# Performance work log

Measured on AMD Instinct MI355X. Metric: run time of the kernel, lower is better.

Reference implementation:

```python
import jax, jax.numpy as jnp
import numpy as np

EPS_PROJ = 4e-3   # geoopt float32 ball projection eps
ATANH_EPS = 1e-7

def artanh(x):
    return jnp.arctanh(jnp.clip(x, -1.0 + ATANH_EPS, 1.0 - ATANH_EPS))

def project(x):
    norm = jnp.linalg.norm(x, axis=-1, keepdims=True)
    maxnorm = 1.0 - EPS_PROJ
    return jnp.where(norm > maxnorm, x * (maxnorm / jnp.maximum(norm, 1e-15)), x)

def expmap0(u):
    un = jnp.linalg.norm(u, axis=-1, keepdims=True)
    return jnp.tanh(un) * u / jnp.maximum(un, 1e-15)

def mobius_add(x, y):
    x2 = jnp.sum(x * x, -1, keepdims=True)
    y2 = jnp.sum(y * y, -1, keepdims=True)
    xy = jnp.sum(x * y, -1, keepdims=True)
    num = (1 + 2 * xy + y2) * x + (1 - x2) * y
    den = 1 + 2 * xy + x2 * y2
    return num / jnp.maximum(den, 1e-15)

def mobius_matvec(W, x):
    xn = jnp.linalg.norm(x, axis=-1, keepdims=True)
    mx = x @ W.T
    mxn = jnp.linalg.norm(mx, axis=-1, keepdims=True)
    res = jnp.tanh(mxn / jnp.maximum(xn, 1e-15) * artanh(xn)) * (mx / jnp.maximum(mxn, 1e-15))
    return jnp.where(mxn == 0, jnp.zeros_like(res), res)

def mobius_linear(x, W, b):
    # hyperbolic_input=True, hyperbolic bias, nonlin=None
    return project(mobius_add(mobius_matvec(W, x), b))

def mobius_scalar_mul(r, t):
    tn = jnp.linalg.norm(t, axis=-1, keepdims=True)
    return jnp.tanh(r * artanh(tn)) * (t / jnp.maximum(tn, 1e-15))

def pair_dist(ht, hs):
    # Poincare dist (c=1): 2*artanh(||(-x) mobius_add y||); closed form via GEMM
    x2 = jnp.sum(ht * ht, -1)                    # (b,t)
    y2 = jnp.sum(hs * hs, -1)                    # (b,s)
    xy = jnp.einsum('btd,bsd->bts', ht, hs)      # (b,t,s)
    diff2 = jnp.maximum(x2[:, :, None] + y2[:, None, :] - 2 * xy, 0.0)
    den = jnp.maximum(1 - 2 * xy + x2[:, :, None] * y2[:, None, :], 1e-15)
    return 2.0 * artanh(jnp.sqrt(diff2 / den))


def setup_inputs() -> dict:
    key = jax.random.key(0)
    ks = jax.random.split(key, 7)
    B, T, S, D = 8, 2048, 2048, 128
    source = project(expmap0(0.5 * jax.random.normal(ks[0], (B, T, D), jnp.float32)))
    memory_bank = project(expmap0(0.5 * jax.random.normal(ks[1], (B, S, D), jnp.float32)))
    W_out = 0.01 * jax.random.normal(ks[2], (D, 2 * D), jnp.float32)
    b_out = expmap0(0.25 * jax.random.normal(ks[3], (D,), jnp.float32))
    beta_w = 0.01 * jax.random.normal(ks[4], (1, 1), jnp.float32)
    beta_b = expmap0(0.25 * jax.random.normal(ks[5], (1,), jnp.float32))
    memory_lengths = jax.random.randint(ks[6], (B,), S // 2, S + 1).astype(jnp.int64)
    return {"source": source, "memory_bank": memory_bank, "W_out": W_out,
            "b_out": b_out, "beta_w": beta_w, "beta_b": beta_b,
            "memory_lengths": memory_lengths}


def reference(source, memory_bank, W_out, b_out, beta_w, beta_b, memory_lengths):
    B, T, D = source.shape
    S = memory_bank.shape[1]
    # --- score: -beta(dist(h_t_i, h_s_j)) over all (i,j), vectorized ---
    d = pair_dist(source, memory_bank)[..., None]        # (b,t,s,1)
    align = -mobius_linear(d, beta_w, beta_b)[..., 0]     # (b,t,s)
    # --- length masking ---
    mask = jnp.arange(S) < memory_lengths[:, None]        # (b,s)
    align = jnp.where(mask[:, None, :], align, -jnp.inf)
    align_vectors = jax.nn.softmax(align, axis=-1)        # (b,t,s)
    # --- mobius weighted midpoint over src dim (reducedim=[2]) ---
    y2 = jnp.sum(memory_bank * memory_bank, -1)           # (b,s)
    gamma = 2.0 / jnp.maximum(1.0 - y2, 1e-15)            # lambda_x, k=-1
    den = jnp.einsum('bts,bs->bt', align_vectors, gamma - 1.0)
    den = jnp.where(den >= 0, jnp.maximum(den, 1e-10), jnp.minimum(den, -1e-10))
    nom = jnp.einsum('bts,bs,bsd->btd', align_vectors, gamma, memory_bank)
    cvec = mobius_scalar_mul(0.5, nom / den[..., None])   # (b,t,d)
    # --- output mobius linear on concat, attn_type='hype' => no tanh ---
    concat_c = jnp.concatenate([cvec, source], axis=-1)   # (b,t,2d)
    attn_h = mobius_linear(concat_c, W_out, b_out)        # (b,t,d)
    return attn_h.transpose(1, 0, 2), align_vectors.transpose(1, 0, 2)
```

## Files before the change

### kernel.cpp

```cpp
#include <hip/hip_runtime.h>
#include <stdint.h>

#define B_ 8
#define T_ 2048
#define S_ 2048
#define D_ 128
#define CAP_ 1024

typedef __attribute__((ext_vector_type(8))) short short8;
typedef __attribute__((ext_vector_type(4))) float f32x4;

#define MAXN_ (1.0f - 0.004f)
#define CLIP1_ 0.99999988f

__device__ __forceinline__ unsigned short f2bf(float f) {
    unsigned int u = __builtin_bit_cast(unsigned int, f);
    u += 0x7fffu + ((u >> 16) & 1u);
    return (unsigned short)(u >> 16);
}
__device__ __forceinline__ unsigned int pack2(float a, float b) {
    return (unsigned int)f2bf(a) | ((unsigned int)f2bf(b) << 16);
}
__device__ __forceinline__ float bf2f(unsigned short u) {
    return __builtin_bit_cast(float, ((unsigned int)u) << 16);
}
__device__ __forceinline__ float tanh_fast(float x) {
    float e = __expf(-2.f * fabsf(x));
    float r = (1.f - e) / (1.f + e);
    return copysignf(r, x);
}
__device__ __forceinline__ float atanh_clip(float x) {
    x = fminf(x, CLIP1_);
    return 0.5f * __logf((1.f + x) / (1.f - x));
}
__device__ __forceinline__ float ep_from_av(float av, float w, float bbs, float b2s) {
    float mv = tanh_fast(w * av);
    float ab = mv * bbs;
    float m2 = mv * mv;
    float num = (1.f + 2.f * ab + b2s) * mv + (1.f - m2) * bbs;
    float dd2 = 1.f + 2.f * ab + m2 * b2s;
    float ma = num / fmaxf(dd2, 1e-15f);
    float am = fabsf(ma);
    if (am > MAXN_) ma = ma * (MAXN_ / fmaxf(am, 1e-15f));
    return __expf(-ma);
}
__device__ __forceinline__ float sat_ep(float w, float bbs) {
    return ep_from_av(atanh_clip(2.f), w, bbs, bbs * bbs);
}
__device__ __forceinline__ int get_len(const int* mlen, int b) {
    int is64 = (mlen[1] == 0);
    return is64 ? mlen[2 * b] : mlen[b];
}

__global__ __launch_bounds__(256) void k_prep(
    const float* __restrict__ src, const float* __restrict__ mem,
    const float* __restrict__ Wout, const int* __restrict__ mlen,
    unsigned short* __restrict__ srcb, unsigned short* __restrict__ memb,
    float* __restrict__ x2a, float* __restrict__ y2a,
    unsigned short* __restrict__ Wb, float* __restrict__ Gbase,
    float* __restrict__ nombase)
{
    __shared__ unsigned short cc_l[128][128];
    __shared__ float gam_l[128];
    __shared__ float gm1_l[128];
    __shared__ float nb_l[2][128];

    const int bid = blockIdx.x;
    const int tid = threadIdx.x;

    if (bid < 256) {
        const bool ismem = bid >= 128;
        const float* inp = ismem ? mem : src;
        unsigned short* outp = ismem ? memb : srcb;
        float* na = ismem ? y2a : x2a;
        const int row0 = (bid & 127) * 128;
        const int lr = tid >> 1;
        const int r = row0 + lr;
        const int ch = (tid & 1) * 64;

        float4 v[16];
        float sq = 0.f;
        const float* rp = inp + (size_t)r * D_ + ch;
        #pragma unroll
        for (int i = 0; i < 16; ++i) {
            v[i] = *(const float4*)(rp + 4 * i);
            sq += v[i].x * v[i].x + v[i].y * v[i].y + v[i].z * v[i].z + v[i].w * v[i].w;
        }
        sq += __shfl_xor(sq, 1);
        unsigned short* op = outp + (size_t)r * D_ + ch;
        #pragma unroll
        for (int i = 0; i < 8; ++i) {
            uint4 pk;
            pk.x = pack2(v[2 * i].x, v[2 * i].y);
            pk.y = pack2(v[2 * i].z, v[2 * i].w);
            pk.z = pack2(v[2 * i + 1].x, v[2 * i + 1].y);
            pk.w = pack2(v[2 * i + 1].z, v[2 * i + 1].w);
            *(uint4*)(op + 8 * i) = pk;
            if (ismem) *(uint4*)&cc_l[lr][ch + 8 * i] = pk;
        }
        if ((tid & 1) == 0) {
            na[r] = sq;
            if (ismem) {
                int b = r >> 11;
                int lenb = get_len(mlen, b);
                bool vld = (r & 2047) < lenb;
                float gam = vld ? 2.f / fmaxf(1.f - sq, 1e-15f) : 0.f;
                gam_l[lr] = gam;
                gm1_l[lr] = vld ? (gam - 1.f) : 0.f;
            }
        }
        if (ismem) {
            __syncthreads();
            const int b = row0 >> 11;
            const int c = tid & 127;
            const int h = tid >> 7;
            float acc = 0.f;
            #pragma unroll 8
            for (int r2 = h * 64; r2 < h * 64 + 64; ++r2)
                acc += gam_l[r2] * bf2f(cc_l[r2][c]);
            nb_l[h][c] = acc;
            __syncthreads();
            if (tid < 128)
                atomicAdd(&nombase[b * D_ + tid], nb_l[0][tid] + nb_l[1][tid]);
            if (tid < 64) {
                float g = gm1_l[tid] + gm1_l[tid + 64];
                g += __shfl_xor(g, 1); g += __shfl_xor(g, 2);
                g += __shfl_xor(g, 4); g += __shfl_xor(g, 8);
                g += __shfl_xor(g, 16); g += __shfl_xor(g, 32);
                if (tid == 0) atomicAdd(&Gbase[b], g);
            }
        }
    } else {
        const int idx0 = (bid - 256) * 4096 + tid * 16;
        float4 v0 = *(const float4*)(Wout + idx0);
        float4 v1 = *(const float4*)(Wout + idx0 + 4);
        float4 v2 = *(const float4*)(Wout + idx0 + 8);
        float4 v3 = *(const float4*)(Wout + idx0 + 12);
        uint4 p0, p1;
        p0.x = pack2(v0.x, v0.y); p0.y = pack2(v0.z, v0.w);
        p0.z = pack2(v1.x, v1.y); p0.w = pack2(v1.z, v1.w);
        p1.x = pack2(v2.x, v2.y); p1.y = pack2(v2.z, v2.w);
        p1.z = pack2(v3.x, v3.y); p1.w = pack2(v3.z, v3.w);
        *(uint4*)(Wb + idx0) = p0;
        *(uint4*)(Wb + idx0 + 8) = p1;
    }
}

__global__ __launch_bounds__(256, 2) void k_score(
    const unsigned short* __restrict__ srcb, const unsigned short* __restrict__ memb,
    const float* __restrict__ x2a, const float* __restrict__ y2a,
    const float* __restrict__ bw, const float* __restrict__ bbp,
    const int* __restrict__ mlen,
    unsigned int* __restrict__ cnt, unsigned int* __restrict__ listR,
    unsigned int* __restrict__ listS, float* __restrict__ listEp,
    float* __restrict__ alignp)
{
    __shared__ unsigned short xs[128][136];
    __shared__ unsigned short ys[128][136];
    __shared__ float x2s[128], y2s[128];

    const int tid = threadIdx.x;
    const int blk = blockIdx.x;
    const int b = blk & 7;
    const int rr = blk >> 3;
    const int tt = rr & 15;
    const int st = rr >> 4;
    const int t0 = tt * 128, s0 = st * 128;
    const int lane = tid & 63, wave = tid >> 6;
    const int l15 = lane & 15, q = lane >> 4;
    const int wr = wave >> 1, wc = wave & 1;

    const unsigned short* xg = srcb + ((size_t)(b * T_ + t0)) * D_;
    const unsigned short* yg = memb + ((size_t)(b * S_ + s0)) * D_;
    #pragma unroll
    for (int i = 0; i < 8; ++i) {
        int c = i * 256 + tid;
        int row = c >> 4, off = (c & 15) * 8;
        *(uint4*)&xs[row][off] = *(const uint4*)(xg + (size_t)c * 8);
        *(uint4*)&ys[row][off] = *(const uint4*)(yg + (size_t)c * 8);
    }
    if (tid < 128) { x2s[tid] = x2a[b * T_ + t0 + tid]; y2s[tid] = y2a[b * S_ + s0 + tid]; }
    __syncthreads();

    f32x4 acc[4][4];
    #pragma unroll
    for (int m = 0; m < 4; ++m)
        #pragma unroll
        for (int n = 0; n < 4; ++n)
            acc[m][n] = (f32x4){0.f, 0.f, 0.f, 0.f};

    #pragma unroll
    for (int ki = 0; ki < 4; ++ki) {
        short8 af[4], bf[4];
        #pragma unroll
        for (int m = 0; m < 4; ++m)
            af[m] = *(const short8*)&xs[wr * 64 + m * 16 + l15][ki * 32 + q * 8];
        #pragma unroll
        for (int n = 0; n < 4; ++n)
            bf[n] = *(const short8*)&ys[wc * 64 + n * 16 + l15][ki * 32 + q * 8];
        #pragma unroll
        for (int m = 0; m < 4; ++m)
            #pragma unroll
            for (int n = 0; n < 4; ++n)
                acc[m][n] = __builtin_amdgcn_mfma_f32_16x16x32_bf16(af[m], bf[n], acc[m][n], 0, 0, 0);
    }

    const int lenb = get_len(mlen, b);
    const float pv = 1.f / (float)lenb;

    #pragma unroll
    for (int i = 0; i < 16; ++i) {
        int idx = i * 256 + tid;
        int row = idx >> 5;
        int sg = s0 + (idx & 31) * 4;
        float4 o;
        o.x = (sg + 0 < lenb) ? pv : 0.f;
        o.y = (sg + 1 < lenb) ? pv : 0.f;
        o.z = (sg + 2 < lenb) ? pv : 0.f;
        o.w = (sg + 3 < lenb) ? pv : 0.f;
        *(float4*)(alignp + (((size_t)((t0 + row) * 8 + b)) << 11) + sg) = o;
    }

    float us = tanh_fast(0.5f * CLIP1_);
    const float RSAT = us * us;
    float x2r[16];
    #pragma unroll
    for (int m = 0; m < 4; ++m)
        #pragma unroll
        for (int rg = 0; rg < 4; ++rg)
            x2r[m * 4 + rg] = x2s[wr * 64 + m * 16 + q * 4 + rg];

    unsigned long long um = 0ull;
    #pragma unroll
    for (int n = 0; n < 4; ++n) {
        int col = wc * 64 + n * 16 + l15;
        bool valid = (s0 + col) < lenb;
        float y2v = y2s[col];
        #pragma unroll
        for (int m = 0; m < 4; ++m) {
            #pragma unroll
            for (int rg = 0; rg < 4; ++rg) {
                float xy = acc[m][n][rg];
                float x2v = x2r[m * 4 + rg];
                float diff2 = x2v + y2v - 2.f * xy;
                float dden = fmaf(x2v, y2v, 1.f) - 2.f * xy;
                bool unsat = valid && (diff2 < RSAT * dden);
                um |= ((unsigned long long)unsat) << (n * 16 + m * 4 + rg);
            }
        }
    }

    if (__ballot(um != 0ull)) {
        const float w = bw[0];
        const float bbs = bbp[0];
        const float b2s = bbs * bbs;
        for (int n = 0; n < 4; ++n) {
            int col = wc * 64 + n * 16 + l15;
            float y2v = y2s[col];
            for (int m = 0; m < 4; ++m) {
                for (int rg = 0; rg < 4; ++rg) {
                    if (!(um & (1ull << (n * 16 + m * 4 + rg)))) continue;
                    int row = wr * 64 + m * 16 + q * 4 + rg;
                    float xy = acc[m][n][rg];
                    float x2v = x2r[m * 4 + rg];
                    float diff2 = fmaxf(x2v + y2v - 2.f * xy, 0.f);
                    float dden = fmaxf(fmaf(x2v, y2v, 1.f) - 2.f * xy, 1e-15f);
                    float u = fminf(sqrtf(diff2 / dden), CLIP1_);
                    float dp = __logf((1.f + u) / (1.f - u));
                    float ep = ep_from_av(atanh_clip(dp), w, bbs, b2s);
                    int rix = b * T_ + t0 + row;
                    unsigned int idx = atomicAdd(cnt, 1u);
                    if (idx < CAP_) {
                        listR[idx] = (unsigned int)rix;
                        listS[idx] = (unsigned int)(b * S_ + s0 + col);
                        listEp[idx] = ep;
                    }
                    (void)y2v;
                }
            }
        }
    }
}

__global__ __launch_bounds__(256, 1) void k_out(
    const float* __restrict__ src, const float* __restrict__ mem,
    const unsigned short* __restrict__ Wb, const float* __restrict__ bvec,
    const float* __restrict__ bw, const float* __restrict__ bbp,
    const int* __restrict__ mlen, const float* __restrict__ Gbase,
    const float* __restrict__ nombase, const float* __restrict__ y2a,
    const unsigned int* __restrict__ cnt, const unsigned int* __restrict__ listR,
    const unsigned int* __restrict__ listS, const float* __restrict__ listEp,
    float* __restrict__ attnp)
{
    __shared__ unsigned short W_l[128][264];
    __shared__ unsigned short cc_l[64][264];
    __shared__ float b_l[128];
    __shared__ float nomn2_l[64], srcn2_l[64], cs_l[64], xn_l[64];
    __shared__ float redA[64], redB[64];
    __shared__ float fA_l[64], fB_l[64];
    __shared__ float bb2_l;

    const int tid = threadIdx.x;
    const int b = blockIdx.x & 7;
    const int tt = blockIdx.x >> 3;
    const int t0 = tt * 64;
    const int lane = tid & 63;
    const int wave = tid >> 6;
    const int l15 = lane & 15;
    const int q = lane >> 4;

    const float epsat = sat_ep(bw[0], bbp[0]);
    const int lenb = get_len(mlen, b);
    unsigned int nc = *cnt; if (nc > CAP_) nc = CAP_;

    #pragma unroll
    for (int i = 0; i < 16; ++i) {
        int c = i * 256 + tid;
        int row = c >> 5, off = (c & 31) * 8;
        *(uint4*)&W_l[row][off] = *(const uint4*)(Wb + (size_t)c * 8);
    }
    if (tid < 128) b_l[tid] = bvec[tid];
    if (tid < 64) { redA[tid] = 0.f; redB[tid] = 0.f; }

    const int r_s = tid >> 2;
    const int d0 = (tid & 3) * 32;
    float4 nv[8], sv[8];
    {
        #pragma unroll
        for (int i = 0; i < 8; ++i) {
            float4 nb = *(const float4*)(nombase + b * D_ + d0 + 4 * i);
            nv[i].x = epsat * nb.x; nv[i].y = epsat * nb.y;
            nv[i].z = epsat * nb.z; nv[i].w = epsat * nb.w;
        }
        if (nc) {
            int myrix = b * T_ + t0 + r_s;
            for (unsigned int i = 0; i < nc; ++i) {
                if ((int)listR[i] != myrix) continue;
                unsigned int sg = listS[i];
                float y2v = y2a[sg];
                float gam = 2.f / fmaxf(1.f - y2v, 1e-15f);
                float cg = (listEp[i] - epsat) * gam;
                const float* yrow = mem + (size_t)sg * D_ + d0;
                #pragma unroll
                for (int k2 = 0; k2 < 8; ++k2) {
                    float4 yv = *(const float4*)(yrow + 4 * k2);
                    nv[k2].x += cg * yv.x; nv[k2].y += cg * yv.y;
                    nv[k2].z += cg * yv.z; nv[k2].w += cg * yv.w;
                }
            }
        }
        size_t sbase = ((size_t)(b * T_ + t0 + r_s)) * D_ + d0;
        float nn = 0.f, ss = 0.f;
        #pragma unroll
        for (int i = 0; i < 8; ++i) {
            sv[i] = *(const float4*)(src + sbase + 4 * i);
            nn += nv[i].x * nv[i].x + nv[i].y * nv[i].y + nv[i].z * nv[i].z + nv[i].w * nv[i].w;
            ss += sv[i].x * sv[i].x + sv[i].y * sv[i].y + sv[i].z * sv[i].z + sv[i].w * sv[i].w;
        }
        nn += __shfl_xor(nn, 1); nn += __shfl_xor(nn, 2);
        ss += __shfl_xor(ss, 1); ss += __shfl_xor(ss, 2);
        if ((tid & 3) == 0) { nomn2_l[r_s] = nn; srcn2_l[r_s] = ss; }
    }
    __syncthreads();

    if (tid == 255) {
        float s = 0.f;
        for (int j = 0; j < 128; ++j) s += b_l[j] * b_l[j];
        bb2_l = s;
    }
    if (tid < 64) {
        int myrix = b * T_ + t0 + tid;
        float Lv = epsat * (float)lenb;
        float Gv = epsat * Gbase[b];
        if (nc) {
            for (unsigned int i = 0; i < nc; ++i) {
                if ((int)listR[i] != myrix) continue;
                float dep = listEp[i] - epsat;
                float y2v = y2a[listS[i]];
                float gam = 2.f / fmaxf(1.f - y2v, 1e-15f);
                Lv += dep;
                Gv += dep * (gam - 1.f);
            }
        }
        float dv = Gv / Lv;
        dv = (dv >= 0.f) ? fmaxf(dv, 1e-10f) : fminf(dv, -1e-10f);
        float Z = Lv * dv;
        float nn2 = nomn2_l[tid];
        float tn = sqrtf(nn2) / fabsf(Z);
        float f = tanh_fast(0.5f * atanh_clip(tn));
        float cs = f / (fmaxf(tn, 1e-15f) * Z);
        cs_l[tid] = cs;
        xn_l[tid] = sqrtf(cs * cs * nn2 + srcn2_l[tid]);
    }
    __syncthreads();

    {
        float cs = cs_l[r_s];
        #pragma unroll
        for (int i = 0; i < 8; ++i) {
            uint2 pk;
            pk.x = pack2(nv[i].x * cs, nv[i].y * cs);
            pk.y = pack2(nv[i].z * cs, nv[i].w * cs);
            *(uint2*)&cc_l[r_s][d0 + 4 * i] = pk;
            uint2 ps;
            ps.x = pack2(sv[i].x, sv[i].y);
            ps.y = pack2(sv[i].z, sv[i].w);
            *(uint2*)&cc_l[r_s][128 + d0 + 4 * i] = ps;
        }
    }
    __syncthreads();

    f32x4 acc[4][2];
    #pragma unroll
    for (int m = 0; m < 4; ++m)
        #pragma unroll
        for (int n = 0; n < 2; ++n)
            acc[m][n] = (f32x4){0.f, 0.f, 0.f, 0.f};
    #pragma unroll
    for (int ki = 0; ki < 8; ++ki) {
        short8 af[4], bf[2];
        #pragma unroll
        for (int m = 0; m < 4; ++m)
            af[m] = *(const short8*)&cc_l[m * 16 + l15][ki * 32 + q * 8];
        #pragma unroll
        for (int n = 0; n < 2; ++n)
            bf[n] = *(const short8*)&W_l[wave * 32 + n * 16 + l15][ki * 32 + q * 8];
        #pragma unroll
        for (int m = 0; m < 4; ++m)
            #pragma unroll
            for (int n = 0; n < 2; ++n)
                acc[m][n] = __builtin_amdgcn_mfma_f32_16x16x32_bf16(af[m], bf[n], acc[m][n], 0, 0, 0);
    }

    float bj[2];
    #pragma unroll
    for (int n = 0; n < 2; ++n) bj[n] = b_l[wave * 32 + n * 16 + l15];

    #pragma unroll
    for (int m = 0; m < 4; ++m) {
        #pragma unroll
        for (int rg = 0; rg < 4; ++rg) {
            int row = m * 16 + q * 4 + rg;
            float pA = 0.f, pB = 0.f;
            #pragma unroll
            for (int n = 0; n < 2; ++n) {
                float v = acc[m][n][rg];
                pA += v * v;
                pB += v * bj[n];
            }
            pA += __shfl_xor(pA, 1); pB += __shfl_xor(pB, 1);
            pA += __shfl_xor(pA, 2); pB += __shfl_xor(pB, 2);
            pA += __shfl_xor(pA, 4); pB += __shfl_xor(pB, 4);
            pA += __shfl_xor(pA, 8); pB += __shfl_xor(pB, 8);
            if (l15 == 0) {
                atomicAdd(&redA[row], pA);
                atomicAdd(&redB[row], pB);
            }
        }
    }
    __syncthreads();

    if (tid < 64) {
        float mxn2 = redA[tid];
        float mxb = redB[tid];
        float xn = xn_l[tid];
        float atx = atanh_clip(xn);
        float mxn = sqrtf(mxn2);
        float scg = tanh_fast(mxn / fmaxf(xn, 1e-15f) * atx) / fmaxf(mxn, 1e-15f);
        float res2 = scg * scg * mxn2;
        float xyb = scg * mxb;
        float b2v = bb2_l;
        float c1 = 1.f + 2.f * xyb + b2v;
        float c2 = 1.f - res2;
        float dd = fmaxf(1.f + 2.f * xyb + res2 * b2v, 1e-15f);
        float nn = sqrtf(fmaxf(c1 * c1 * res2 + 2.f * c1 * c2 * xyb + c2 * c2 * b2v, 0.f)) / dd;
        float rho = (nn > MAXN_) ? (MAXN_ / fmaxf(nn, 1e-15f)) : 1.f;
        fA_l[tid] = rho * c1 * scg / dd;
        fB_l[tid] = rho * c2 / dd;
    }
    __syncthreads();

    #pragma unroll
    for (int m = 0; m < 4; ++m) {
        #pragma unroll
        for (int n = 0; n < 2; ++n) {
            int col = wave * 32 + n * 16 + l15;
            #pragma unroll
            for (int rg = 0; rg < 4; ++rg) {
                int row = m * 16 + q * 4 + rg;
                attnp[((size_t)((t0 + row) * 8 + b)) * D_ + col] =
                    fA_l[row] * acc[m][n][rg] + fB_l[row] * b_l[col];
            }
        }
    }
}

__global__ __launch_bounds__(256) void k_fix(
    const float* __restrict__ bw, const float* __restrict__ bbp,
    const int* __restrict__ mlen, const unsigned int* __restrict__ cnt,
    const unsigned int* __restrict__ listR, const unsigned int* __restrict__ listS,
    const float* __restrict__ listEp, float* __restrict__ alignp)
{
    unsigned int n = *cnt;
    if (n > CAP_) n = CAP_;
    if (n == 0) return;
    const float epsat = sat_ep(bw[0], bbp[0]);
    for (unsigned int i = 0; i < n; ++i) {
        unsigned int rix = listR[i];
        int b = rix >> 11, t = rix & 2047;
        int lenb = get_len(mlen, b);
        float L = epsat * (float)lenb;
        for (unsigned int j = 0; j < n; ++j)
            if (listR[j] == rix) L += listEp[j] - epsat;
        float pvv = epsat / L;
        size_t base = ((size_t)(t * 8 + b)) << 11;
        for (int s = threadIdx.x; s < S_; s += 256)
            alignp[base + s] = (s < lenb) ? pvv : 0.f;
    }
    __syncthreads();
    for (unsigned int i = threadIdx.x; i < n; i += 256) {
        unsigned int rix = listR[i];
        int b = rix >> 11, t = rix & 2047;
        unsigned int s = listS[i] & 2047;
        int lenb = get_len(mlen, b);
        float L = epsat * (float)lenb;
        for (unsigned int j = 0; j < n; ++j)
            if (listR[j] == rix) L += listEp[j] - epsat;
        alignp[(((size_t)(t * 8 + b)) << 11) + s] = listEp[i] / L;
    }
}

extern "C" void kernel_launch(void* const* d_in, const int* in_sizes, int n_in,
                              void* d_out, int out_size, void* d_ws, size_t ws_size,
                              hipStream_t stream) {
    const float* src  = (const float*)d_in[0];
    const float* mem  = (const float*)d_in[1];
    const float* Wout = (const float*)d_in[2];
    const float* bvec = (const float*)d_in[3];
    const float* bw   = (const float*)d_in[4];
    const float* bb   = (const float*)d_in[5];
    const int*   mlen = (const int*)d_in[6];

    float* attnp  = (float*)d_out;
    float* alignp = attnp + (size_t)T_ * B_ * D_;
    unsigned short* srcb = (unsigned short*)d_out;
    unsigned short* memb = (unsigned short*)d_out + (size_t)B_ * T_ * D_;

    float* ws_f = (float*)d_ws;
    unsigned int* cnt   = (unsigned int*)d_ws;
    float* Gbase        = ws_f + 8;
    float* nombase      = ws_f + 32;
    unsigned int* listR = (unsigned int*)(ws_f + 2048);
    unsigned int* listS = (unsigned int*)(ws_f + 3072);
    float* listEp       = ws_f + 4096;
    float* x2a          = ws_f + 8192;
    float* y2a          = ws_f + 24576;
    unsigned short* Wb  = (unsigned short*)(ws_f + 40960);

    hipMemsetAsync(d_ws, 0, 4608, stream);
    hipLaunchKernelGGL(k_prep, dim3(264), dim3(256), 0, stream,
                       src, mem, Wout, mlen, srcb, memb, x2a, y2a, Wb, Gbase, nombase);
    hipLaunchKernelGGL(k_score, dim3(2048), dim3(256), 0, stream,
                       srcb, memb, x2a, y2a, bw, bb, mlen,
                       cnt, listR, listS, listEp, alignp);
    hipLaunchKernelGGL(k_out, dim3(256), dim3(256), 0, stream,
                       src, mem, Wb, bvec, bw, bb, mlen, Gbase, nombase, y2a,
                       cnt, listR, listS, listEp, attnp);
    hipLaunchKernelGGL(k_fix, dim3(1), dim3(256), 0, stream,
                       bw, bb, mlen, cnt, listR, listS, listEp, alignp);
}
```

Measured before the change: 197.3 us.

## Drop memset and fix kernel, use per-block partials and contiguous align writes

Per-block partial sums replace the global atomics for nombase and Gbase. The consumer kernel reduces those partials, so the workspace memset is no longer needed, and the counter is zeroed inside k_prep instead. The separate single-block fix-up kernel is folded into block 0 of k_out, which removes one launch. The uniform align fill in k_score now writes one contiguous 64KB region per block, placed before the MFMA loop, instead of strided 512B row segments. The cost is some extra reduction work in k_out and serial fix-up work on one block.

```diff
diff --git a/kernel.cpp b/kernel.cpp
--- a/kernel.cpp
+++ b/kernel.cpp
@@ -57,8 +57,8 @@
     const float* __restrict__ Wout, const int* __restrict__ mlen,
     unsigned short* __restrict__ srcb, unsigned short* __restrict__ memb,
     float* __restrict__ x2a, float* __restrict__ y2a,
-    unsigned short* __restrict__ Wb, float* __restrict__ Gbase,
-    float* __restrict__ nombase)
+    unsigned short* __restrict__ Wb, float* __restrict__ gpart,
+    float* __restrict__ nbpart, unsigned int* __restrict__ cnt)
 {
     __shared__ unsigned short cc_l[128][128];
     __shared__ float gam_l[128];
@@ -111,7 +111,7 @@
         }
         if (ismem) {
             __syncthreads();
-            const int b = row0 >> 11;
+            const int slot = bid - 128;
             const int c = tid & 127;
             const int h = tid >> 7;
             float acc = 0.f;
@@ -121,16 +121,17 @@
             nb_l[h][c] = acc;
             __syncthreads();
             if (tid < 128)
-                atomicAdd(&nombase[b * D_ + tid], nb_l[0][tid] + nb_l[1][tid]);
+                nbpart[slot * 128 + tid] = nb_l[0][tid] + nb_l[1][tid];
             if (tid < 64) {
                 float g = gm1_l[tid] + gm1_l[tid + 64];
                 g += __shfl_xor(g, 1); g += __shfl_xor(g, 2);
                 g += __shfl_xor(g, 4); g += __shfl_xor(g, 8);
                 g += __shfl_xor(g, 16); g += __shfl_xor(g, 32);
-                if (tid == 0) atomicAdd(&Gbase[b], g);
+                if (tid == 0) gpart[slot] = g;
             }
         }
     } else {
+        if (bid == 256 && tid == 0) *cnt = 0u;
         const int idx0 = (bid - 256) * 4096 + tid * 16;
         float4 v0 = *(const float4*)(Wout + idx0);
         float4 v1 = *(const float4*)(Wout + idx0 + 4);
@@ -158,6 +159,8 @@
     __shared__ unsigned short xs[128][136];
     __shared__ unsigned short ys[128][136];
     __shared__ float x2s[128], y2s[128];
+    __shared__ int len_l[8];
+    __shared__ float pv_l[8];
 
     const int tid = threadIdx.x;
     const int blk = blockIdx.x;
@@ -180,7 +183,31 @@
         *(uint4*)&ys[row][off] = *(const uint4*)(yg + (size_t)c * 8);
     }
     if (tid < 128) { x2s[tid] = x2a[b * T_ + t0 + tid]; y2s[tid] = y2a[b * S_ + s0 + tid]; }
-    __syncthreads();
+    if (tid < 8) {
+        int lv = get_len(mlen, tid);
+        len_l[tid] = lv;
+        pv_l[tid] = 1.f / (float)lv;
+    }
+    __syncthreads();
+
+    {
+        const int base_f4 = blk * 4096;
+        #pragma unroll
+        for (int i = 0; i < 16; ++i) {
+            int f4 = base_f4 + i * 256 + tid;
+            int r = f4 >> 9;
+            int b2 = r & 7;
+            int s4 = (f4 & 511) << 2;
+            int lv = len_l[b2];
+            float pvv = pv_l[b2];
+            float4 o;
+            o.x = (s4 + 0 < lv) ? pvv : 0.f;
+            o.y = (s4 + 1 < lv) ? pvv : 0.f;
+            o.z = (s4 + 2 < lv) ? pvv : 0.f;
+            o.w = (s4 + 3 < lv) ? pvv : 0.f;
+            *(float4*)(alignp + (size_t)f4 * 4) = o;
+        }
+    }
 
     f32x4 acc[4][4];
     #pragma unroll
@@ -205,21 +232,7 @@
                 acc[m][n] = __builtin_amdgcn_mfma_f32_16x16x32_bf16(af[m], bf[n], acc[m][n], 0, 0, 0);
     }
 
-    const int lenb = get_len(mlen, b);
-    const float pv = 1.f / (float)lenb;
-
-    #pragma unroll
-    for (int i = 0; i < 16; ++i) {
-        int idx = i * 256 + tid;
-        int row = idx >> 5;
-        int sg = s0 + (idx & 31) * 4;
-        float4 o;
-        o.x = (sg + 0 < lenb) ? pv : 0.f;
-        o.y = (sg + 1 < lenb) ? pv : 0.f;
-        o.z = (sg + 2 < lenb) ? pv : 0.f;
-        o.w = (sg + 3 < lenb) ? pv : 0.f;
-        *(float4*)(alignp + (((size_t)((t0 + row) * 8 + b)) << 11) + sg) = o;
-    }
+    const int lenb = len_l[b];
 
     float us = tanh_fast(0.5f * CLIP1_);
     const float RSAT = us * us;
@@ -256,13 +269,13 @@
         const float b2s = bbs * bbs;
         for (int n = 0; n < 4; ++n) {
             int col = wc * 64 + n * 16 + l15;
-            float y2v = y2s[col];
             for (int m = 0; m < 4; ++m) {
                 for (int rg = 0; rg < 4; ++rg) {
                     if (!(um & (1ull << (n * 16 + m * 4 + rg)))) continue;
                     int row = wr * 64 + m * 16 + q * 4 + rg;
                     float xy = acc[m][n][rg];
                     float x2v = x2r[m * 4 + rg];
+                    float y2v = y2s[col];
                     float diff2 = fmaxf(x2v + y2v - 2.f * xy, 0.f);
                     float dden = fmaxf(fmaf(x2v, y2v, 1.f) - 2.f * xy, 1e-15f);
                     float u = fminf(sqrtf(diff2 / dden), CLIP1_);
@@ -275,7 +288,6 @@
                         listS[idx] = (unsigned int)(b * S_ + s0 + col);
                         listEp[idx] = ep;
                     }
-                    (void)y2v;
                 }
             }
         }
@@ -286,19 +298,20 @@
     const float* __restrict__ src, const float* __restrict__ mem,
     const unsigned short* __restrict__ Wb, const float* __restrict__ bvec,
     const float* __restrict__ bw, const float* __restrict__ bbp,
-    const int* __restrict__ mlen, const float* __restrict__ Gbase,
-    const float* __restrict__ nombase, const float* __restrict__ y2a,
+    const int* __restrict__ mlen, const float* __restrict__ gpart,
+    const float* __restrict__ nbpart, const float* __restrict__ y2a,
     const unsigned int* __restrict__ cnt, const unsigned int* __restrict__ listR,
     const unsigned int* __restrict__ listS, const float* __restrict__ listEp,
-    float* __restrict__ attnp)
+    float* __restrict__ attnp, float* __restrict__ alignp)
 {
     __shared__ unsigned short W_l[128][264];
     __shared__ unsigned short cc_l[64][264];
     __shared__ float b_l[128];
+    __shared__ float nombase_l[128];
     __shared__ float nomn2_l[64], srcn2_l[64], cs_l[64], xn_l[64];
     __shared__ float redA[64], redB[64];
     __shared__ float fA_l[64], fB_l[64];
-    __shared__ float bb2_l;
+    __shared__ float bb2_l, Gb_l;
 
     const int tid = threadIdx.x;
     const int b = blockIdx.x & 7;
@@ -321,6 +334,24 @@
     }
     if (tid < 128) b_l[tid] = bvec[tid];
     if (tid < 64) { redA[tid] = 0.f; redB[tid] = 0.f; }
+    if (tid < 128) {
+        float s = 0.f;
+        #pragma unroll
+        for (int j = 0; j < 16; ++j) s += nbpart[(b * 16 + j) * 128 + tid];
+        nombase_l[tid] = s;
+    }
+    if (tid == 128) {
+        float g = 0.f;
+        #pragma unroll
+        for (int j = 0; j < 16; ++j) g += gpart[b * 16 + j];
+        Gb_l = g;
+    }
+    if (tid == 129) {
+        float s = 0.f;
+        for (int j = 0; j < 128; ++j) { float v = bvec[j]; s += v * v; }
+        bb2_l = s;
+    }
+    __syncthreads();
 
     const int r_s = tid >> 2;
     const int d0 = (tid & 3) * 32;
@@ -328,9 +359,10 @@
     {
         #pragma unroll
         for (int i = 0; i < 8; ++i) {
-            float4 nb = *(const float4*)(nombase + b * D_ + d0 + 4 * i);
-            nv[i].x = epsat * nb.x; nv[i].y = epsat * nb.y;
-            nv[i].z = epsat * nb.z; nv[i].w = epsat * nb.w;
+            nv[i].x = epsat * nombase_l[d0 + 4 * i + 0];
+            nv[i].y = epsat * nombase_l[d0 + 4 * i + 1];
+            nv[i].z = epsat * nombase_l[d0 + 4 * i + 2];
+            nv[i].w = epsat * nombase_l[d0 + 4 * i + 3];
         }
         if (nc) {
             int myrix = b * T_ + t0 + r_s;
@@ -363,15 +395,10 @@
     }
     __syncthreads();
 
-    if (tid == 255) {
-        float s = 0.f;
-        for (int j = 0; j < 128; ++j) s += b_l[j] * b_l[j];
-        bb2_l = s;
-    }
     if (tid < 64) {
         int myrix = b * T_ + t0 + tid;
         float Lv = epsat * (float)lenb;
-        float Gv = epsat * Gbase[b];
+        float Gv = epsat * Gb_l;
         if (nc) {
             for (unsigned int i = 0; i < nc; ++i) {
                 if ((int)listR[i] != myrix) continue;
@@ -493,40 +520,31 @@
             }
         }
     }
-}
-
-__global__ __launch_bounds__(256) void k_fix(
-    const float* __restrict__ bw, const float* __restrict__ bbp,
-    const int* __restrict__ mlen, const unsigned int* __restrict__ cnt,
-    const unsigned int* __restrict__ listR, const unsigned int* __restrict__ listS,
-    const float* __restrict__ listEp, float* __restrict__ alignp)
-{
-    unsigned int n = *cnt;
-    if (n > CAP_) n = CAP_;
-    if (n == 0) return;
-    const float epsat = sat_ep(bw[0], bbp[0]);
-    for (unsigned int i = 0; i < n; ++i) {
-        unsigned int rix = listR[i];
-        int b = rix >> 11, t = rix & 2047;
-        int lenb = get_len(mlen, b);
-        float L = epsat * (float)lenb;
-        for (unsigned int j = 0; j < n; ++j)
-            if (listR[j] == rix) L += listEp[j] - epsat;
-        float pvv = epsat / L;
-        size_t base = ((size_t)(t * 8 + b)) << 11;
-        for (int s = threadIdx.x; s < S_; s += 256)
-            alignp[base + s] = (s < lenb) ? pvv : 0.f;
-    }
-    __syncthreads();
-    for (unsigned int i = threadIdx.x; i < n; i += 256) {
-        unsigned int rix = listR[i];
-        int b = rix >> 11, t = rix & 2047;
-        unsigned int s = listS[i] & 2047;
-        int lenb = get_len(mlen, b);
-        float L = epsat * (float)lenb;
-        for (unsigned int j = 0; j < n; ++j)
-            if (listR[j] == rix) L += listEp[j] - epsat;
-        alignp[(((size_t)(t * 8 + b)) << 11) + s] = listEp[i] / L;
+
+    if (blockIdx.x == 0 && nc > 0) {
+        for (unsigned int i = 0; i < nc; ++i) {
+            unsigned int rix = listR[i];
+            int fb = rix >> 11, ft = rix & 2047;
+            int flen = get_len(mlen, fb);
+            float L = epsat * (float)flen;
+            for (unsigned int j = 0; j < nc; ++j)
+                if (listR[j] == rix) L += listEp[j] - epsat;
+            float pvv = epsat / L;
+            size_t base = ((size_t)(ft * 8 + fb)) << 11;
+            for (int s = tid; s < S_; s += 256)
+                alignp[base + s] = (s < flen) ? pvv : 0.f;
+        }
+        __syncthreads();
+        for (unsigned int i = tid; i < nc; i += 256) {
+            unsigned int rix = listR[i];
+            int fb = rix >> 11, ft = rix & 2047;
+            unsigned int s = listS[i] & 2047;
+            int flen = get_len(mlen, fb);
+            float L = epsat * (float)flen;
+            for (unsigned int j = 0; j < nc; ++j)
+                if (listR[j] == rix) L += listEp[j] - epsat;
+            alignp[(((size_t)(ft * 8 + fb)) << 11) + s] = listEp[i] / L;
+        }
     }
 }
 
@@ -548,24 +566,22 @@
 
     float* ws_f = (float*)d_ws;
     unsigned int* cnt   = (unsigned int*)d_ws;
-    float* Gbase        = ws_f + 8;
-    float* nombase      = ws_f + 32;
-    unsigned int* listR = (unsigned int*)(ws_f + 2048);
-    unsigned int* listS = (unsigned int*)(ws_f + 3072);
-    float* listEp       = ws_f + 4096;
-    float* x2a          = ws_f + 8192;
-    float* y2a          = ws_f + 24576;
-    unsigned short* Wb  = (unsigned short*)(ws_f + 40960);
-
-    hipMemsetAsync(d_ws, 0, 4608, stream);
+    float* gpart        = ws_f + 8;
+    float* nbpart       = ws_f + 1024;
+    unsigned int* listR = (unsigned int*)(ws_f + 20480);
+    unsigned int* listS = (unsigned int*)(ws_f + 21504);
+    float* listEp       = ws_f + 22528;
+    float* x2a          = ws_f + 24576;
+    float* y2a          = ws_f + 40960;
+    unsigned short* Wb  = (unsigned short*)(ws_f + 57344);
+
     hipLaunchKernelGGL(k_prep, dim3(264), dim3(256), 0, stream,
-                       src, mem, Wout, mlen, srcb, memb, x2a, y2a, Wb, Gbase, nombase);
+                       src, mem, Wout, mlen, srcb, memb, x2a, y2a, Wb,
+                       gpart, nbpart, cnt);
     hipLaunchKernelGGL(k_score, dim3(2048), dim3(256), 0, stream,
                        srcb, memb, x2a, y2a, bw, bb, mlen,
                        cnt, listR, listS, listEp, alignp);
     hipLaunchKernelGGL(k_out, dim3(256), dim3(256), 0, stream,
-                       src, mem, Wb, bvec, bw, bb, mlen, Gbase, nombase, y2a,
-                       cnt, listR, listS, listEp, attnp);
-    hipLaunchKernelGGL(k_fix, dim3(1), dim3(256), 0, stream,
-                       bw, bb, mlen, cnt, listR, listS, listEp, alignp);
-}
+                       src, mem, Wb, bvec, bw, bb, mlen, gpart, nbpart, y2a,
+                       cnt, listR, listS, listEp, attnp, alignp);
+}
```

Result: no change. 193.8 us (-1.8%).
